# Kernel optimization log

Hardware: AMD Instinct MI355X
Metric: run time of the kernel (lower is better)

Reference implementation:

```python
import jax, jax.numpy as jnp
import numpy as np

# Standard SMPL kinematic tree (24 joints), parent of joint i
PARENTS = np.array([-1, 0, 0, 0, 1, 2, 3, 4, 5, 6, 7, 8, 9, 9, 9,
                    12, 13, 14, 16, 17, 18, 19, 20, 21])
N_JOINTS = 24
EPS = 1e-8  # stands in for the tiny gaussian eps the torch code adds


def rodrigues(r):
    """Axis-angle (N,3) -> rotation matrices (N,3,3)."""
    theta = jnp.linalg.norm(r, axis=1, keepdims=True) + EPS        # (N,1)
    r_hat = r / theta                                              # (N,3)
    cos = jnp.cos(theta)[..., None]                                # (N,1,1)
    sin = jnp.sin(theta)[..., None]
    z = jnp.zeros_like(r_hat[:, 0])
    # skew-symmetric cross-product matrix of r_hat
    m = jnp.stack([z, -r_hat[:, 2], r_hat[:, 1],
                   r_hat[:, 2], z, -r_hat[:, 0],
                   -r_hat[:, 1], r_hat[:, 0], z], axis=1).reshape(-1, 3, 3)
    outer = r_hat[:, :, None] * r_hat[:, None, :]                  # (N,3,3)
    eye = jnp.eye(3, dtype=r.dtype)
    return cos * eye + (1.0 - cos) * outer + sin * m


def setup_inputs() -> dict:
    key = jax.random.key(0)
    k0, k1, k2, k3, k4 = jax.random.split(key, 5)
    B, V, J = 512, 6890, N_JOINTS
    return {
        "T_hat": jax.random.normal(k0, (V, 3), dtype=jnp.float32),
        "J_hat": jax.random.normal(k1, (J, 3), dtype=jnp.float32),
        "weights": jax.random.uniform(k2, (V, J), dtype=jnp.float32),
        "pose": jax.random.normal(k3, (B, J * 3), dtype=jnp.float32),
        "trans": jax.random.normal(k4, (B, 3), dtype=jnp.float32),
    }


def reference(T_hat, J_hat, weights, pose, trans):
    B = pose.shape[0]
    dt = pose.dtype
    # per-joint rotation matrices: (B,24,3,3)
    R = rodrigues(pose.reshape(-1, 3)).reshape(B, N_JOINTS, 3, 3)

    # relative joint offsets along the tree (24,3)
    rel_J = jnp.concatenate([J_hat[:1], J_hat[1:] - J_hat[PARENTS[1:]]], axis=0)

    # local SE(3) transforms (B,24,4,4)
    top = jnp.concatenate(
        [R, jnp.broadcast_to(rel_J[None, :, :, None], (B, N_JOINTS, 3, 1))],
        axis=-1)                                                   # (B,24,3,4)
    bottom = jnp.broadcast_to(
        jnp.array([0.0, 0.0, 0.0, 1.0], dtype=dt), (B, N_JOINTS, 1, 4))
    G_local = jnp.concatenate([top, bottom], axis=2)               # (B,24,4,4)

    # forward kinematics along the fixed 24-joint tree (small fixed loop)
    results = [G_local[:, 0]]
    for i in range(1, N_JOINTS):
        results.append(jnp.matmul(results[PARENTS[i]], G_local[:, i]))
    G = jnp.stack(results, axis=1)                                 # (B,24,4,4)

    # remove rest-pose joint locations from the translation column
    Jh = jnp.concatenate(
        [J_hat, jnp.zeros((N_JOINTS, 1), dtype=dt)], axis=1)       # (24,4)
    corr = jnp.einsum('bjxy,jy->bjx', G, Jh)                       # (B,24,4)
    G = G.at[:, :, :, 3].add(-corr)

    # linear blend skinning: per-vertex blended transforms (B,V,4,4)
    T = jnp.einsum('bjxy,vj->bvxy', G, weights)
    vh = jnp.concatenate(
        [T_hat, jnp.ones((T_hat.shape[0], 1), dtype=dt)], axis=1)  # (V,4)
    v = jnp.einsum('bvxy,vy->bvx', T, vh)[..., :3]                 # (B,V,3)
    return v + trans[:, None, :]
```

## Files before the change

kernel.cpp:

```cpp
#include <hip/hip_runtime.h>
#include <math.h>

#define NJ 24
#define TPB 256
#define BPT 8
#define FK_BPB 8

typedef _Float16 f16x8 __attribute__((ext_vector_type(8)));
typedef float f32x4 __attribute__((ext_vector_type(4)));

__device__ __constant__ int PAR[NJ] = {-1,0,0,0,1,2,3,4,5,6,7,8,9,9,9,12,13,14,16,17,18,19,20,21};
__device__ __constant__ int CHAIN[NJ][9] = {
  {0,-1,-1,-1,-1,-1,-1,-1,-1},
  {0, 1,-1,-1,-1,-1,-1,-1,-1},
  {0, 2,-1,-1,-1,-1,-1,-1,-1},
  {0, 3,-1,-1,-1,-1,-1,-1,-1},
  {0, 1, 4,-1,-1,-1,-1,-1,-1},
  {0, 2, 5,-1,-1,-1,-1,-1,-1},
  {0, 3, 6,-1,-1,-1,-1,-1,-1},
  {0, 1, 4, 7,-1,-1,-1,-1,-1},
  {0, 2, 5, 8,-1,-1,-1,-1,-1},
  {0, 3, 6, 9,-1,-1,-1,-1,-1},
  {0, 1, 4, 7,10,-1,-1,-1,-1},
  {0, 2, 5, 8,11,-1,-1,-1,-1},
  {0, 3, 6, 9,12,-1,-1,-1,-1},
  {0, 3, 6, 9,13,-1,-1,-1,-1},
  {0, 3, 6, 9,14,-1,-1,-1,-1},
  {0, 3, 6, 9,12,15,-1,-1,-1},
  {0, 3, 6, 9,13,16,-1,-1,-1},
  {0, 3, 6, 9,14,17,-1,-1,-1},
  {0, 3, 6, 9,13,16,18,-1,-1},
  {0, 3, 6, 9,14,17,19,-1,-1},
  {0, 3, 6, 9,13,16,18,20,-1},
  {0, 3, 6, 9,14,17,19,21,-1},
  {0, 3, 6, 9,13,16,18,20,22},
  {0, 3, 6, 9,14,17,19,21,23},
};


__device__ __forceinline__ void fk_local(const float* __restrict__ J_hat,
                                         const float* __restrict__ pose,
                                         int b, int j, float* __restrict__ L )
{
  const float rx = pose[b * 72 + j * 3 + 0];
  const float ry = pose[b * 72 + j * 3 + 1];
  const float rz = pose[b * 72 + j * 3 + 2];
  const float theta = sqrtf(rx * rx + ry * ry + rz * rz) + 1e-8f;
  const float inv = 1.0f / theta;
  const float ux = rx * inv, uy = ry * inv, uz = rz * inv;
  const float c = cosf(theta), s = sinf(theta);
  const float ic = 1.0f - c;

  float tx = J_hat[j * 3 + 0];
  float ty = J_hat[j * 3 + 1];
  float tz = J_hat[j * 3 + 2];
  const int p = PAR[j];
  if (p >= 0) {
    tx -= J_hat[p * 3 + 0];
    ty -= J_hat[p * 3 + 1];
    tz -= J_hat[p * 3 + 2];
  }

  L[0]  = c + ic * ux * ux;
  L[1]  = ic * ux * uy - s * uz;
  L[2]  = ic * ux * uz + s * uy;
  L[3]  = tx;
  L[4]  = ic * uy * ux + s * uz;
  L[5]  = c + ic * uy * uy;
  L[6]  = ic * uy * uz - s * ux;
  L[7]  = ty;
  L[8]  = ic * uz * ux - s * uy;
  L[9]  = ic * uz * uy + s * ux;
  L[10] = c + ic * uz * uz;
  L[11] = tz;
}

__device__ __forceinline__ void fk_compose(const float (*__restrict__ Lc)[12],
                                           const float* __restrict__ J_hat,
                                           int j, float* __restrict__ g )
{
#pragma unroll
  for (int k = 0; k < 12; k++) g[k] = Lc[0][k];
#pragma unroll
  for (int d = 1; d < 9; d++) {
    const int a = CHAIN[j][d];
    if (a >= 0) {
      float l[12];
#pragma unroll
      for (int k = 0; k < 12; k++) l[k] = Lc[a][k];
      float n[12];
#pragma unroll
      for (int r = 0; r < 3; r++) {
        const float gr0 = g[r * 4 + 0], gr1 = g[r * 4 + 1], gr2 = g[r * 4 + 2];
        n[r * 4 + 0] = gr0 * l[0] + gr1 * l[4] + gr2 * l[8];
        n[r * 4 + 1] = gr0 * l[1] + gr1 * l[5] + gr2 * l[9];
        n[r * 4 + 2] = gr0 * l[2] + gr1 * l[6] + gr2 * l[10];
        n[r * 4 + 3] = gr0 * l[3] + gr1 * l[7] + gr2 * l[11] + g[r * 4 + 3];
      }
#pragma unroll
      for (int k = 0; k < 12; k++) g[k] = n[k];
    }
  }
  const float jx = J_hat[j * 3 + 0], jy = J_hat[j * 3 + 1], jz = J_hat[j * 3 + 2];
  g[3]  -= g[0] * jx + g[1] * jy + g[2]  * jz;
  g[7]  -= g[4] * jx + g[5] * jy + g[6]  * jz;
  g[11] -= g[8] * jx + g[9] * jy + g[10] * jz;
}


__global__ __launch_bounds__(TPB) void smpl_prep_wh(
    const float* __restrict__ weights, _Float16* __restrict__ W_h, int V, int VP)
{
  const int v = blockIdx.x * TPB + threadIdx.x;
  if (v >= VP) return;
  _Float16 row[32];
#pragma unroll
  for (int k = 0; k < 32; k++) row[k] = (_Float16)0.f;
  if (v < V) {
    const float4* wp = reinterpret_cast<const float4*>(weights + (size_t)v * 24);
#pragma unroll
    for (int q = 0; q < 6; q++) {
      const float4 t = wp[q];
      row[q * 4 + 0] = (_Float16)t.x;
      row[q * 4 + 1] = (_Float16)t.y;
      row[q * 4 + 2] = (_Float16)t.z;
      row[q * 4 + 3] = (_Float16)t.w;
    }
  }
  float4* dst = reinterpret_cast<float4*>(W_h + (size_t)v * 32);
  const float4* src = reinterpret_cast<const float4*>(row);
#pragma unroll
  for (int q = 0; q < 4; q++) dst[q] = src[q];
}

__global__ __launch_bounds__(FK_BPB * 32) void smpl_fk_gh(
    const float* __restrict__ J_hat,
    const float* __restrict__ pose,
    _Float16* __restrict__ G_hT,
    int B)
{
  __shared__ __align__(16) float Lc[FK_BPB][NJ][12];
  const int lb = threadIdx.x >> 5;
  const int j  = threadIdx.x & 31;
  const int b  = blockIdx.x * FK_BPB + lb;
  const bool compute = (j < NJ) && (b < B);

  if (compute) {
    float L[12];
    fk_local(J_hat, pose, b, j, L);
#pragma unroll
    for (int k = 0; k < 12; k++) Lc[lb][j][k] = L[k];
  }
  __syncthreads();

  float g[12];
#pragma unroll
  for (int k = 0; k < 12; k++) g[k] = 0.0f;
  if (compute) fk_compose(Lc[lb], J_hat, j, g);

  if (b < B) {
    _Float16* dst = G_hT + (size_t)b * 512;
#pragma unroll
    for (int c = 0; c < 16; c++) {
      _Float16 val = (_Float16)0.f;
      if (j < NJ && c < 12) val = (_Float16)g[c];
      dst[c * 32 + j] = val;
    }
  }
}

__global__ __launch_bounds__(TPB) void smpl_blend_mfma(
    const float* __restrict__ T_hat,
    const _Float16* __restrict__ W_h,
    const float* __restrict__ trans,
    const _Float16* __restrict__ G_hT,
    float* __restrict__ out,
    int V)
{
  __shared__ __align__(16) float Cbuf[4][16 * 72];

  const int tid  = threadIdx.x;
  const int wid  = tid >> 6;
  const int lane = tid & 63;
  const int vbase = blockIdx.x * 256 + wid * 64;
  const int b0 = blockIdx.y * BPT;

  const int fr = lane & 15;
  const int kb = lane >> 4;

  f16x8 afrag[4];
#pragma unroll
  for (int t = 0; t < 4; t++)
    afrag[t] = *reinterpret_cast<const f16x8*>(
        W_h + ((size_t)(vbase + t * 16 + fr)) * 32 + kb * 8);

  f16x8 bfrag[BPT];
#pragma unroll
  for (int bi = 0; bi < BPT; bi++)
    bfrag[bi] = *reinterpret_cast<const f16x8*>(
        G_hT + ((size_t)(b0 + bi) * 16 + fr) * 32 + kb * 8);

  const int myv = vbase + lane;
  float x = 0.f, y = 0.f, z = 0.f;
  if (myv < V) {
    x = T_hat[myv * 3 + 0];
    y = T_hat[myv * 3 + 1];
    z = T_hat[myv * 3 + 2];
  }

  float* __restrict__ cb = &Cbuf[wid][0];
  const int wrow = (lane >> 4) * 4;

#pragma unroll
  for (int bi = 0; bi < BPT; bi++) {
    const int b = b0 + bi;

#pragma unroll
    for (int t = 0; t < 4; t++) {
      f32x4 acc = {0.f, 0.f, 0.f, 0.f};
      acc = __builtin_amdgcn_mfma_f32_16x16x32_f16(afrag[t], bfrag[bi], acc, 0, 0, 0);
      *reinterpret_cast<f32x4*>(cb + fr * 72 + t * 16 + wrow) = acc;
    }

    float c[12];
#pragma unroll
    for (int q = 0; q < 12; q++) c[q] = cb[q * 72 + lane];

    if (myv < V) {
      const float t0 = trans[b * 3 + 0];
      const float t1 = trans[b * 3 + 1];
      const float t2 = trans[b * 3 + 2];
      float* op = out + ((size_t)b * V + myv) * 3;
      op[0] = c[0] * x + c[1] * y + c[2]  * z + c[3]  + t0;
      op[1] = c[4] * x + c[5] * y + c[6]  * z + c[7]  + t1;
      op[2] = c[8] * x + c[9] * y + c[10] * z + c[11] + t2;
    }
  }
}


__global__ __launch_bounds__(FK_BPB * 32) void smpl_fk_kernel(
    const float* __restrict__ J_hat,
    const float* __restrict__ pose,
    float* __restrict__ Gws, int B)
{
  __shared__ __align__(16) float Lc[FK_BPB][NJ][12];
  const int lb = threadIdx.x >> 5;
  const int j  = threadIdx.x & 31;
  const int b  = blockIdx.x * FK_BPB + lb;
  const bool active = (j < NJ) && (b < B);

  if (active) {
    float L[12];
    fk_local(J_hat, pose, b, j, L);
#pragma unroll
    for (int k = 0; k < 12; k++) Lc[lb][j][k] = L[k];
  }
  __syncthreads();
  if (active) {
    float g[12];
    fk_compose(Lc[lb], J_hat, j, g);
    float* dst = Gws + (size_t)b * (NJ * 12) + j * 12;
#pragma unroll
    for (int k = 0; k < 12; k++) dst[k] = g[k];
  }
}

__global__ __launch_bounds__(TPB) void smpl_blend_ws_kernel(
    const float* __restrict__ T_hat,
    const float* __restrict__ weights,
    const float* __restrict__ trans,
    const float* __restrict__ Gws,
    float* __restrict__ out, int V)
{
  __shared__ __align__(16) float4 Gs[4 * NJ * 3];

  const int b0 = blockIdx.y * 4;
  const int tid = threadIdx.x;
  {
    const float4* src = reinterpret_cast<const float4*>(Gws + (size_t)b0 * (NJ * 12));
    Gs[tid] = src[tid];
    if (tid < 4 * NJ * 3 - TPB) Gs[TPB + tid] = src[TPB + tid];
  }
  __syncthreads();

  const int v = blockIdx.x * TPB + tid;
  if (v >= V) return;

  float w[24];
  const float4* wp = reinterpret_cast<const float4*>(weights + (size_t)v * 24);
#pragma unroll
  for (int q = 0; q < 6; q++) {
    const float4 t = wp[q];
    w[q * 4 + 0] = t.x; w[q * 4 + 1] = t.y;
    w[q * 4 + 2] = t.z; w[q * 4 + 3] = t.w;
  }
  const float x = T_hat[v * 3 + 0];
  const float y = T_hat[v * 3 + 1];
  const float z = T_hat[v * 3 + 2];

#pragma unroll 1
  for (int bi = 0; bi < 4; bi++) {
    const int b = b0 + bi;
    const float4* __restrict__ Gb = &Gs[bi * NJ * 3];
    float acc[12];
#pragma unroll
    for (int j = 0; j < NJ; j++) {
      const float4 g0 = Gb[j * 3 + 0];
      const float4 g1 = Gb[j * 3 + 1];
      const float4 g2 = Gb[j * 3 + 2];
      const float wj = w[j];
      if (j == 0) {
        acc[0]  = wj * g0.x;  acc[1]  = wj * g0.y;
        acc[2]  = wj * g0.z;  acc[3]  = wj * g0.w;
        acc[4]  = wj * g1.x;  acc[5]  = wj * g1.y;
        acc[6]  = wj * g1.z;  acc[7]  = wj * g1.w;
        acc[8]  = wj * g2.x;  acc[9]  = wj * g2.y;
        acc[10] = wj * g2.z;  acc[11] = wj * g2.w;
      } else {
        acc[0]  = fmaf(wj, g0.x, acc[0]);
        acc[1]  = fmaf(wj, g0.y, acc[1]);
        acc[2]  = fmaf(wj, g0.z, acc[2]);
        acc[3]  = fmaf(wj, g0.w, acc[3]);
        acc[4]  = fmaf(wj, g1.x, acc[4]);
        acc[5]  = fmaf(wj, g1.y, acc[5]);
        acc[6]  = fmaf(wj, g1.z, acc[6]);
        acc[7]  = fmaf(wj, g1.w, acc[7]);
        acc[8]  = fmaf(wj, g2.x, acc[8]);
        acc[9]  = fmaf(wj, g2.y, acc[9]);
        acc[10] = fmaf(wj, g2.z, acc[10]);
        acc[11] = fmaf(wj, g2.w, acc[11]);
      }
    }
    const float t0 = trans[b * 3 + 0];
    const float t1 = trans[b * 3 + 1];
    const float t2 = trans[b * 3 + 2];
    float* op = out + ((size_t)b * V + v) * 3;
    op[0] = acc[0] * x + acc[1] * y + acc[2]  * z + acc[3]  + t0;
    op[1] = acc[4] * x + acc[5] * y + acc[6]  * z + acc[7]  + t1;
    op[2] = acc[8] * x + acc[9] * y + acc[10] * z + acc[11] + t2;
  }
}

__global__ __launch_bounds__(TPB) void smpl_blend_lds_kernel(
    const float* __restrict__ T_hat,
    const float* __restrict__ J_hat,
    const float* __restrict__ weights,
    const float* __restrict__ pose,
    const float* __restrict__ trans,
    float* __restrict__ out, int V)
{
  __shared__ __align__(16) float Lc[NJ][12];
  __shared__ __align__(16) float Gm[NJ][12];
  const int b = blockIdx.y;
  const int tid = threadIdx.x;

  if (tid < NJ) {
    float L[12];
    fk_local(J_hat, pose, b, tid, L);
#pragma unroll
    for (int k = 0; k < 12; k++) Lc[tid][k] = L[k];
  }
  __syncthreads();
  if (tid < NJ) {
    float g[12];
    fk_compose(Lc, J_hat, tid, g);
#pragma unroll
    for (int k = 0; k < 12; k++) Gm[tid][k] = g[k];
  }
  __syncthreads();

  const int v = blockIdx.x * TPB + tid;
  if (v >= V) return;

  float acc[12];
#pragma unroll
  for (int k = 0; k < 12; k++) acc[k] = 0.0f;
  const float* wv = weights + (size_t)v * 24;
#pragma unroll
  for (int j = 0; j < NJ; j++) {
    const float wj = wv[j];
#pragma unroll
    for (int k = 0; k < 12; k++) acc[k] = fmaf(wj, Gm[j][k], acc[k]);
  }
  const float x = T_hat[v * 3 + 0], y = T_hat[v * 3 + 1], z = T_hat[v * 3 + 2];
  float* op = out + ((size_t)b * V + v) * 3;
  op[0] = acc[0] * x + acc[1] * y + acc[2]  * z + acc[3]  + trans[b * 3 + 0];
  op[1] = acc[4] * x + acc[5] * y + acc[6]  * z + acc[7]  + trans[b * 3 + 1];
  op[2] = acc[8] * x + acc[9] * y + acc[10] * z + acc[11] + trans[b * 3 + 2];
}

extern "C" void kernel_launch(void* const* d_in, const int* in_sizes, int n_in,
                              void* d_out, int out_size, void* d_ws, size_t ws_size,
                              hipStream_t stream) {
  const float* T_hat   = (const float*)d_in[0];
  const float* J_hat   = (const float*)d_in[1];
  const float* weights = (const float*)d_in[2];
  const float* pose    = (const float*)d_in[3];
  const float* trans   = (const float*)d_in[4];
  float* out = (float*)d_out;

  const int V = in_sizes[0] / 3;
  const int B = in_sizes[3] / 72;

  const int nvchunks = (V + 255) / 256;
  const int VP = nvchunks * 256;

  const size_t wh_bytes = (size_t)VP * 32 * sizeof(_Float16);
  const size_t gh_bytes = (size_t)B * 512 * sizeof(_Float16);
  const size_t mfma_need = wh_bytes + gh_bytes;
  const size_t ws8_need  = (size_t)B * NJ * 12 * sizeof(float);

  if (ws_size >= mfma_need && (B % BPT) == 0 && (B % FK_BPB) == 0) {
    _Float16* W_h  = (_Float16*)d_ws;
    _Float16* G_hT = (_Float16*)((char*)d_ws + wh_bytes);

    smpl_prep_wh<<<nvchunks, TPB, 0, stream>>>(weights, W_h, V, VP);
    smpl_fk_gh<<<B / FK_BPB, FK_BPB * 32, 0, stream>>>(J_hat, pose, G_hT, B);
    dim3 grid(nvchunks, B / BPT);
    smpl_blend_mfma<<<grid, TPB, 0, stream>>>(T_hat, W_h, trans, G_hT, out, V);
  } else if (ws_size >= ws8_need && (B % 4) == 0) {
    float* Gws = (float*)d_ws;
    smpl_fk_kernel<<<(B + FK_BPB - 1) / FK_BPB, FK_BPB * 32, 0, stream>>>(J_hat, pose, Gws, B);
    dim3 grid(nvchunks, B / 4);
    smpl_blend_ws_kernel<<<grid, TPB, 0, stream>>>(T_hat, weights, trans, Gws, out, V);
  } else {
    dim3 grid(nvchunks, B);
    smpl_blend_lds_kernel<<<grid, TPB, 0, stream>>>(T_hat, J_hat, weights, pose, trans, out, V);
  }
}
```

Before: 34.54 us.

## Merge prep kernels and swap MFMA operands to drop LDS transpose in blend

The weight-conversion and forward-kinematics prep kernels are merged into one launch whose blocks branch on block index, removing one kernel launch. In the blend kernel the MFMA operands are swapped so each lane's accumulator holds one row of a vertex's blended transform, which is then applied to that vertex's rest position directly. This removes the per-wave LDS buffer and its store/reload round trip. Each lane now writes one output component, giving a more scattered store pattern and idling a quarter of the lanes on the final write.

```diff
diff --git a/kernel.cpp b/kernel.cpp
--- a/kernel.cpp
+++ b/kernel.cpp
@@ -108,63 +108,65 @@
 }
 
 
-__global__ __launch_bounds__(TPB) void smpl_prep_wh(
-    const float* __restrict__ weights, _Float16* __restrict__ W_h, int V, int VP)
-{
-  const int v = blockIdx.x * TPB + threadIdx.x;
-  if (v >= VP) return;
-  _Float16 row[32];
-#pragma unroll
-  for (int k = 0; k < 32; k++) row[k] = (_Float16)0.f;
-  if (v < V) {
-    const float4* wp = reinterpret_cast<const float4*>(weights + (size_t)v * 24);
-#pragma unroll
-    for (int q = 0; q < 6; q++) {
-      const float4 t = wp[q];
-      row[q * 4 + 0] = (_Float16)t.x;
-      row[q * 4 + 1] = (_Float16)t.y;
-      row[q * 4 + 2] = (_Float16)t.z;
-      row[q * 4 + 3] = (_Float16)t.w;
-    }
-  }
-  float4* dst = reinterpret_cast<float4*>(W_h + (size_t)v * 32);
-  const float4* src = reinterpret_cast<const float4*>(row);
-#pragma unroll
-  for (int q = 0; q < 4; q++) dst[q] = src[q];
-}
-
-__global__ __launch_bounds__(FK_BPB * 32) void smpl_fk_gh(
+__global__ __launch_bounds__(TPB) void smpl_prep_all(
+    const float* __restrict__ weights,
     const float* __restrict__ J_hat,
     const float* __restrict__ pose,
+    _Float16* __restrict__ W_h,
     _Float16* __restrict__ G_hT,
-    int B)
+    int V, int VP, int nvchunks, int B)
 {
   __shared__ __align__(16) float Lc[FK_BPB][NJ][12];
-  const int lb = threadIdx.x >> 5;
-  const int j  = threadIdx.x & 31;
-  const int b  = blockIdx.x * FK_BPB + lb;
-  const bool compute = (j < NJ) && (b < B);
-
-  if (compute) {
-    float L[12];
-    fk_local(J_hat, pose, b, j, L);
-#pragma unroll
-    for (int k = 0; k < 12; k++) Lc[lb][j][k] = L[k];
-  }
-  __syncthreads();
-
-  float g[12];
-#pragma unroll
-  for (int k = 0; k < 12; k++) g[k] = 0.0f;
-  if (compute) fk_compose(Lc[lb], J_hat, j, g);
-
-  if (b < B) {
-    _Float16* dst = G_hT + (size_t)b * 512;
-#pragma unroll
-    for (int c = 0; c < 16; c++) {
-      _Float16 val = (_Float16)0.f;
-      if (j < NJ && c < 12) val = (_Float16)g[c];
-      dst[c * 32 + j] = val;
+  const int tid = threadIdx.x;
+
+  if ((int)blockIdx.x < nvchunks) {
+    const int v = blockIdx.x * TPB + tid;
+    if (v >= VP) return;
+    _Float16 row[32];
+#pragma unroll
+    for (int k = 0; k < 32; k++) row[k] = (_Float16)0.f;
+    if (v < V) {
+      const float4* wp = reinterpret_cast<const float4*>(weights + (size_t)v * 24);
+#pragma unroll
+      for (int q = 0; q < 6; q++) {
+        const float4 t = wp[q];
+        row[q * 4 + 0] = (_Float16)t.x;
+        row[q * 4 + 1] = (_Float16)t.y;
+        row[q * 4 + 2] = (_Float16)t.z;
+        row[q * 4 + 3] = (_Float16)t.w;
+      }
+    }
+    float4* dst = reinterpret_cast<float4*>(W_h + (size_t)v * 32);
+    const float4* src = reinterpret_cast<const float4*>(row);
+#pragma unroll
+    for (int q = 0; q < 4; q++) dst[q] = src[q];
+  } else {
+    const int lb = tid >> 5;
+    const int j  = tid & 31;
+    const int b  = (blockIdx.x - nvchunks) * FK_BPB + lb;
+    const bool compute = (j < NJ) && (b < B);
+
+    if (compute) {
+      float L[12];
+      fk_local(J_hat, pose, b, j, L);
+#pragma unroll
+      for (int k = 0; k < 12; k++) Lc[lb][j][k] = L[k];
+    }
+    __syncthreads();
+
+    float g[12];
+#pragma unroll
+    for (int k = 0; k < 12; k++) g[k] = 0.0f;
+    if (compute) fk_compose(Lc[lb], J_hat, j, g);
+
+    if (b < B) {
+      _Float16* dst = G_hT + (size_t)b * 512;
+#pragma unroll
+      for (int c = 0; c < 16; c++) {
+        _Float16 val = (_Float16)0.f;
+        if (j < NJ && c < 12) val = (_Float16)g[c];
+        dst[c * 32 + j] = val;
+      }
     }
   }
 }
@@ -177,8 +179,6 @@
     float* __restrict__ out,
     int V)
 {
-  __shared__ __align__(16) float Cbuf[4][16 * 72];
-
   const int tid  = threadIdx.x;
   const int wid  = tid >> 6;
   const int lane = tid & 63;
@@ -188,52 +188,48 @@
   const int fr = lane & 15;
   const int kb = lane >> 4;
 
-  f16x8 afrag[4];
+  f16x8 wfrag[4];
 #pragma unroll
   for (int t = 0; t < 4; t++)
-    afrag[t] = *reinterpret_cast<const f16x8*>(
+    wfrag[t] = *reinterpret_cast<const f16x8*>(
         W_h + ((size_t)(vbase + t * 16 + fr)) * 32 + kb * 8);
 
-  f16x8 bfrag[BPT];
+  f16x8 gfrag[BPT];
 #pragma unroll
   for (int bi = 0; bi < BPT; bi++)
-    bfrag[bi] = *reinterpret_cast<const f16x8*>(
+    gfrag[bi] = *reinterpret_cast<const f16x8*>(
         G_hT + ((size_t)(b0 + bi) * 16 + fr) * 32 + kb * 8);
 
-  const int myv = vbase + lane;
-  float x = 0.f, y = 0.f, z = 0.f;
-  if (myv < V) {
-    x = T_hat[myv * 3 + 0];
-    y = T_hat[myv * 3 + 1];
-    z = T_hat[myv * 3 + 2];
-  }
-
-  float* __restrict__ cb = &Cbuf[wid][0];
-  const int wrow = (lane >> 4) * 4;
+  float thx[4], thy[4], thz[4];
+#pragma unroll
+  for (int t = 0; t < 4; t++) {
+    const int v = vbase + t * 16 + fr;
+    if (v < V) {
+      thx[t] = T_hat[v * 3 + 0];
+      thy[t] = T_hat[v * 3 + 1];
+      thz[t] = T_hat[v * 3 + 2];
+    } else {
+      thx[t] = thy[t] = thz[t] = 0.f;
+    }
+  }
+
+  const int kc = (kb < 3) ? kb : 2;
+  float tsel[BPT];
+#pragma unroll
+  for (int bi = 0; bi < BPT; bi++) tsel[bi] = trans[(b0 + bi) * 3 + kc];
 
 #pragma unroll
   for (int bi = 0; bi < BPT; bi++) {
     const int b = b0 + bi;
-
 #pragma unroll
     for (int t = 0; t < 4; t++) {
       f32x4 acc = {0.f, 0.f, 0.f, 0.f};
-      acc = __builtin_amdgcn_mfma_f32_16x16x32_f16(afrag[t], bfrag[bi], acc, 0, 0, 0);
-      *reinterpret_cast<f32x4*>(cb + fr * 72 + t * 16 + wrow) = acc;
-    }
-
-    float c[12];
-#pragma unroll
-    for (int q = 0; q < 12; q++) c[q] = cb[q * 72 + lane];
-
-    if (myv < V) {
-      const float t0 = trans[b * 3 + 0];
-      const float t1 = trans[b * 3 + 1];
-      const float t2 = trans[b * 3 + 2];
-      float* op = out + ((size_t)b * V + myv) * 3;
-      op[0] = c[0] * x + c[1] * y + c[2]  * z + c[3]  + t0;
-      op[1] = c[4] * x + c[5] * y + c[6]  * z + c[7]  + t1;
-      op[2] = c[8] * x + c[9] * y + c[10] * z + c[11] + t2;
+      acc = __builtin_amdgcn_mfma_f32_16x16x32_f16(gfrag[bi], wfrag[t], acc, 0, 0, 0);
+      const float o = acc[0] * thx[t] + acc[1] * thy[t] + acc[2] * thz[t]
+                    + acc[3] + tsel[bi];
+      const int v = vbase + t * 16 + fr;
+      if (kb < 3 && v < V)
+        out[((size_t)b * V + v) * 3 + kb] = o;
     }
   }
 }
@@ -415,8 +411,9 @@
     _Float16* W_h  = (_Float16*)d_ws;
     _Float16* G_hT = (_Float16*)((char*)d_ws + wh_bytes);
 
-    smpl_prep_wh<<<nvchunks, TPB, 0, stream>>>(weights, W_h, V, VP);
-    smpl_fk_gh<<<B / FK_BPB, FK_BPB * 32, 0, stream>>>(J_hat, pose, G_hT, B);
+    const int prep_blocks = nvchunks + B / FK_BPB;
+    smpl_prep_all<<<prep_blocks, TPB, 0, stream>>>(
+        weights, J_hat, pose, W_h, G_hT, V, VP, nvchunks, B);
     dim3 grid(nvchunks, B / BPT);
     smpl_blend_mfma<<<grid, TPB, 0, stream>>>(T_hat, W_h, trans, G_hT, out, V);
   } else if (ws_size >= ws8_need && (B % 4) == 0) {
```

After: 27.75 us. 1.24x faster.
